# Kernel optimization log

Measured on AMD Instinct MI355X. Metric: run time of the kernel, lower is better.

Reference implementation:

```python
import jax, jax.numpy as jnp
import numpy as np

N = 8192
E = 524288
ALPHA = 0.4


def setup_inputs() -> dict:
    key = jax.random.key(0)
    k1, k2, k3, k4 = jax.random.split(key, 4)
    x = jax.random.normal(k1, (N, 64), dtype=jnp.float32)
    edge_attr = jax.random.uniform(k2, (E,), dtype=jnp.float32)
    row = jax.random.randint(k3, (E,), 0, N)
    col = jax.random.randint(k4, (E,), 0, N)
    edge_index = jnp.stack([row, col]).astype(jnp.int64)
    return {"x": x, "edge_attr": edge_attr, "edge_index": edge_index}


def reference(x, edge_attr, edge_index):
    # PPR diffusion: P = alpha*I + alpha*(1-alpha)*(A + A^2 + A^3)
    # (the theta *= (1-alpha) update in the torch loop is dead: spspmm reuses
    #  the already-scaled previous result, so all power terms share theta1)
    n = x.shape[0]
    row, col = edge_index[0], edge_index[1]
    # degree(col, N): unweighted in-degree count
    deg = jnp.zeros((n,), dtype=x.dtype).at[col].add(jnp.ones((), x.dtype))
    deg_inv_sqrt = deg ** -0.5  # inf at isolated nodes, matching torch pow(-0.5)
    vals = deg_inv_sqrt[row] * edge_attr * deg_inv_sqrt[col]
    # densify normalized adjacency (COO scatter-add == sparse coalesce semantics)
    A = jnp.zeros((n, n), dtype=x.dtype).at[row, col].add(vals)
    theta1 = ALPHA * (1.0 - ALPHA)
    A2 = A @ A      # [N,N]
    A3 = A @ A2     # [N,N]
    P = theta1 * (A + A2 + A3) + ALPHA * jnp.eye(n, dtype=x.dtype)
    return P
```

## Files before the change

### kernel.cpp

```cpp
#include <hip/hip_runtime.h>

#define NN 8192
#define ALPHA  0.4f
#define THETA1 0.24f
#define SLABW  128
#define NSLAB  (NN / SLABW)
#define SLABSZ ((size_t)NN * SLABW)

typedef float    f32x2 __attribute__((ext_vector_type(2)));
typedef float    f32x4 __attribute__((ext_vector_type(4)));
typedef unsigned u32x2 __attribute__((ext_vector_type(2)));

__device__ __forceinline__ unsigned short f2bf(float f) {
    unsigned u = __float_as_uint(f);
    u += 0x7fffu + ((u >> 16) & 1u);
    return (unsigned short)(u >> 16);
}

__global__ __launch_bounds__(256) void deg_count_kernel(const int* __restrict__ row,
                                                        const int* __restrict__ col,
                                                        float* __restrict__ deg,
                                                        int* __restrict__ cnt, int E) {
    int e = blockIdx.x * 256 + threadIdx.x;
    if (e >= E) return;
    unsigned r = (unsigned)row[e], c = (unsigned)col[e];
    if (r < NN && c < NN) {
        atomicAdd(&deg[c], 1.0f);
        atomicAdd(&cnt[r], 1);
    }
}

__global__ __launch_bounds__(256) void scan_kernel(const int* __restrict__ cnt,
                                                   int* __restrict__ rowptr,
                                                   int* __restrict__ cursor) {
    __shared__ int sums[257];
    int t = threadIdx.x;
    int base = t * 32;
    int s = 0;
    for (int j = 0; j < 32; ++j) s += cnt[base + j];
    sums[t] = s;
    __syncthreads();
    if (t == 0) {
        int run = 0;
        for (int i = 0; i < 256; ++i) { int x = sums[i]; sums[i] = run; run += x; }
        sums[256] = run;
    }
    __syncthreads();
    int run = sums[t];
    for (int j = 0; j < 32; ++j) {
        rowptr[base + j] = run;
        cursor[base + j] = run;
        run += cnt[base + j];
    }
    if (t == 255) rowptr[NN] = sums[256];
}

__global__ __launch_bounds__(256) void fill_kernel(const int* __restrict__ row,
                                                   const int* __restrict__ col,
                                                   const float* __restrict__ attr,
                                                   const float* __restrict__ deg,
                                                   int* __restrict__ cursor,
                                                   unsigned* __restrict__ epk,
                                                   float* __restrict__ Af, int E) {
    int e = blockIdx.x * 256 + threadIdx.x;
    if (e >= E) return;
    unsigned r = (unsigned)row[e], c = (unsigned)col[e];
    if (r < NN && c < NN) {
        float v = rsqrtf(deg[r]) * attr[e] * rsqrtf(deg[c]);
        atomicAdd(&Af[(size_t)r * NN + c], v);
        int pos = atomicAdd(&cursor[r], 1);
        epk[pos] = ((unsigned)f2bf(v) << 16) | c;
    }
}

__global__ __launch_bounds__(256) void convert_slab_kernel(const float* __restrict__ in,
                                                           unsigned short* __restrict__ out) {
    int r = blockIdx.x;
    int t = threadIdx.x;
    const float* rowp = in + (size_t)r * NN;
#pragma unroll
    for (int k = 0; k < 8; ++k) {
        int c = k * 1024 + t * 4;
        f32x4 v = __builtin_nontemporal_load((const f32x4*)&rowp[c]);
        unsigned lo = ((unsigned)f2bf(v.y) << 16) | (unsigned)f2bf(v.x);
        unsigned hi = ((unsigned)f2bf(v.w) << 16) | (unsigned)f2bf(v.z);
        u32x2 pk = {lo, hi};
        size_t o = (size_t)(c >> 7) * SLABSZ + (size_t)r * SLABW + (c & 127);
        __builtin_nontemporal_store(pk, (u32x2*)&out[o]);
    }
}

template <int FINAL>
__global__ __launch_bounds__(256) void spmm_kernel(const int* __restrict__ rowptr,
                                                   const unsigned* __restrict__ epk,
                                                   const unsigned short* __restrict__ S,
                                                   unsigned short* __restrict__ OutBf,
                                                   float* __restrict__ P,
                                                   const unsigned short* __restrict__ Abf,
                                                   const unsigned short* __restrict__ A2bf) {
    int lane = threadIdx.x & 63;
    int wave = threadIdx.x >> 6;
    unsigned bid   = blockIdx.x;
    unsigned xcd   = bid & 7u;
    unsigned local = bid >> 3;
    unsigned slab  = (xcd << 3) | (local >> 11);
    unsigned rg    = local & 2047u;
    int r  = (int)(rg * 4 + wave);
    int e0 = __builtin_amdgcn_readfirstlane(rowptr[r]);
    int e1 = __builtin_amdgcn_readfirstlane(rowptr[r + 1]);
    const char* Sc = (const char*)(S + (size_t)slab * SLABSZ) + (lane << 2);
    float a0 = 0.f, a1 = 0.f;

#define GATHER(u) (*(const unsigned*)(Sc + (((size_t)((u) & 0x1fffu)) << 8)))
#define ACCUM(g, u) { float vv = __uint_as_float((u) & 0xffff0000u);        \
                      a0 = fmaf(vv, __uint_as_float((g) << 16), a0);        \
                      a1 = fmaf(vv, __uint_as_float((g) & 0xffff0000u), a1); }
    int e = e0;
    for (; e + 8 <= e1; e += 8) {
        unsigned u0 = epk[e],     u1 = epk[e + 1];
        unsigned u2 = epk[e + 2], u3 = epk[e + 3];
        unsigned u4 = epk[e + 4], u5 = epk[e + 5];
        unsigned u6 = epk[e + 6], u7 = epk[e + 7];
        unsigned g0 = GATHER(u0), g1 = GATHER(u1), g2 = GATHER(u2), g3 = GATHER(u3);
        unsigned g4 = GATHER(u4), g5 = GATHER(u5), g6 = GATHER(u6), g7 = GATHER(u7);
        ACCUM(g0, u0); ACCUM(g1, u1); ACCUM(g2, u2); ACCUM(g3, u3);
        ACCUM(g4, u4); ACCUM(g5, u5); ACCUM(g6, u6); ACCUM(g7, u7);
    }
    for (; e < e1; ++e) {
        unsigned u = epk[e];
        unsigned g = GATHER(u);
        ACCUM(g, u);
    }
#undef GATHER
#undef ACCUM

    int cloc = lane << 1;
    size_t idx_sm = (size_t)slab * SLABSZ + (size_t)r * SLABW + cloc;
    if (FINAL) {
        unsigned ab = __builtin_nontemporal_load((const unsigned*)(Abf + idx_sm));
        unsigned bb = __builtin_nontemporal_load((const unsigned*)(A2bf + idx_sm));
        float o0 = THETA1 * (__uint_as_float(ab << 16) + __uint_as_float(bb << 16) + a0);
        float o1 = THETA1 * (__uint_as_float(ab & 0xffff0000u) + __uint_as_float(bb & 0xffff0000u) + a1);
        int gc = (int)(slab << 7) + cloc;
        int d = r - gc;
        if (d == 0) o0 += ALPHA;
        else if (d == 1) o1 += ALPHA;
        f32x2 o = {o0, o1};
        __builtin_nontemporal_store(o, (f32x2*)(P + (size_t)r * NN + gc));
    } else {
        unsigned pk = ((unsigned)f2bf(a1) << 16) | (unsigned)f2bf(a0);
        __builtin_nontemporal_store(pk, (unsigned*)(OutBf + idx_sm));
    }
}

extern "C" void kernel_launch(void* const* d_in, const int* in_sizes, int n_in,
                              void* d_out, int out_size, void* d_ws, size_t ws_size,
                              hipStream_t stream) {
    const float* attr = (const float*)d_in[1];
    const int*   eidx = (const int*)d_in[2];
    int E = in_sizes[1];
    const int* row = eidx;
    const int* col = eidx + E;

    const size_t MAT = (size_t)NN * NN;
    unsigned short* Abf  = (unsigned short*)d_ws;
    unsigned short* A2bf = Abf + MAT;
    float*    deg    = (float*)(A2bf + MAT);
    int*      cnt    = (int*)(deg + NN);
    int*      rowptr = cnt + NN;
    int*      cursor = rowptr + NN + 2;
    unsigned* epk    = (unsigned*)(cursor + NN);

    size_t need = MAT * 2 * sizeof(unsigned short)
                + (size_t)(NN * 4 + 2) * sizeof(int)
                + (size_t)E * sizeof(unsigned);
    if (ws_size < need) return;

    float* Af = (float*)d_out;
    float* P  = (float*)d_out;

    hipMemsetAsync(d_out, 0, MAT * sizeof(float), stream);
    hipMemsetAsync(deg, 0, NN * sizeof(float), stream);
    hipMemsetAsync(cnt, 0, NN * sizeof(int), stream);

    int eb = (E + 255) / 256;
    deg_count_kernel<<<eb, 256, 0, stream>>>(row, col, deg, cnt, E);
    scan_kernel<<<1, 256, 0, stream>>>(cnt, rowptr, cursor);
    fill_kernel<<<eb, 256, 0, stream>>>(row, col, attr, deg, cursor, epk, Af, E);
    convert_slab_kernel<<<NN, 256, 0, stream>>>(Af, Abf);

    const int SPMM_BLOCKS = 2048 * 64;
    spmm_kernel<0><<<SPMM_BLOCKS, 256, 0, stream>>>(rowptr, epk, Abf, A2bf, nullptr, nullptr, nullptr);
    spmm_kernel<1><<<SPMM_BLOCKS, 256, 0, stream>>>(rowptr, epk, A2bf, nullptr, P, Abf, A2bf);
}
```

Measured before the change: 1.279 ms.

## Factor PPR as A(I+A+A²) via Horner, split edges across half-waves

The first SpMM now writes S2 = I + A + A·A in bf16, and the final pass computes P = theta1·A·S2 + alpha·I. This removes the extra Abf and A2bf reads from the final kernel. Each wave is split into two 32-lane halves that take alternate edges and gather 8-byte chunks, and the halves are combined with a cross-half shuffle. The cost is an extra bf16 rounding of A+A² before the last product, and the upper half-wave is idle during the epilogue.

```diff
diff --git a/kernel.cpp b/kernel.cpp
--- a/kernel.cpp
+++ b/kernel.cpp
@@ -96,8 +96,7 @@
                                                    const unsigned short* __restrict__ S,
                                                    unsigned short* __restrict__ OutBf,
                                                    float* __restrict__ P,
-                                                   const unsigned short* __restrict__ Abf,
-                                                   const unsigned short* __restrict__ A2bf) {
+                                                   const unsigned short* __restrict__ Abf) {
     int lane = threadIdx.x & 63;
     int wave = threadIdx.x >> 6;
     unsigned bid   = blockIdx.x;
@@ -108,48 +107,81 @@
     int r  = (int)(rg * 4 + wave);
     int e0 = __builtin_amdgcn_readfirstlane(rowptr[r]);
     int e1 = __builtin_amdgcn_readfirstlane(rowptr[r + 1]);
-    const char* Sc = (const char*)(S + (size_t)slab * SLABSZ) + (lane << 2);
-    float a0 = 0.f, a1 = 0.f;
-
-#define GATHER(u) (*(const unsigned*)(Sc + (((size_t)((u) & 0x1fffu)) << 8)))
-#define ACCUM(g, u) { float vv = __uint_as_float((u) & 0xffff0000u);        \
-                      a0 = fmaf(vv, __uint_as_float((g) << 16), a0);        \
-                      a1 = fmaf(vv, __uint_as_float((g) & 0xffff0000u), a1); }
-    int e = e0;
-    for (; e + 8 <= e1; e += 8) {
-        unsigned u0 = epk[e],     u1 = epk[e + 1];
-        unsigned u2 = epk[e + 2], u3 = epk[e + 3];
-        unsigned u4 = epk[e + 4], u5 = epk[e + 5];
-        unsigned u6 = epk[e + 6], u7 = epk[e + 7];
-        unsigned g0 = GATHER(u0), g1 = GATHER(u1), g2 = GATHER(u2), g3 = GATHER(u3);
-        unsigned g4 = GATHER(u4), g5 = GATHER(u5), g6 = GATHER(u6), g7 = GATHER(u7);
-        ACCUM(g0, u0); ACCUM(g1, u1); ACCUM(g2, u2); ACCUM(g3, u3);
-        ACCUM(g4, u4); ACCUM(g5, u5); ACCUM(g6, u6); ACCUM(g7, u7);
-    }
-    for (; e < e1; ++e) {
-        unsigned u = epk[e];
-        unsigned g = GATHER(u);
-        ACCUM(g, u);
+    int hiHalf = lane >> 5;
+    int l32 = lane & 31;
+    const char* Sb = (const char*)(S + (size_t)slab * SLABSZ) + (l32 << 3);
+    float a0 = 0.f, a1 = 0.f, a2 = 0.f, a3 = 0.f;
+
+#define GATHER(u) (*(const u32x2*)(Sb + (((size_t)((u) & 0x1fffu)) << 8)))
+#define ACCUM4(g, u) { float vv = __uint_as_float((u) & 0xffff0000u);          \
+    a0 = fmaf(vv, __uint_as_float((g).x << 16), a0);                           \
+    a1 = fmaf(vv, __uint_as_float((g).x & 0xffff0000u), a1);                   \
+    a2 = fmaf(vv, __uint_as_float((g).y << 16), a2);                           \
+    a3 = fmaf(vv, __uint_as_float((g).y & 0xffff0000u), a3); }
+
+    const unsigned* ep = epk + e0;
+    int n = e1 - e0;
+    int npair = n >> 1;
+    int p = 0;
+    for (; p + 8 <= npair; p += 8) {
+        unsigned sel[8];
+#pragma unroll
+        for (int j = 0; j < 8; ++j) {
+            u32x2 q = *(const u32x2*)&ep[2 * (p + j)];
+            sel[j] = hiHalf ? q.y : q.x;
+        }
+        u32x2 g[8];
+#pragma unroll
+        for (int j = 0; j < 8; ++j) g[j] = GATHER(sel[j]);
+#pragma unroll
+        for (int j = 0; j < 8; ++j) ACCUM4(g[j], sel[j]);
+    }
+    for (; p < npair; ++p) {
+        u32x2 q = *(const u32x2*)&ep[2 * p];
+        unsigned s = hiHalf ? q.y : q.x;
+        u32x2 g = GATHER(s);
+        ACCUM4(g, s);
+    }
+    if (n & 1) {
+        unsigned u = ep[n - 1];
+        unsigned s = hiHalf ? 0u : u;
+        u32x2 g = GATHER(s);
+        ACCUM4(g, s);
     }
 #undef GATHER
-#undef ACCUM
-
-    int cloc = lane << 1;
+#undef ACCUM4
+
+    a0 += __shfl_xor(a0, 32);
+    a1 += __shfl_xor(a1, 32);
+    a2 += __shfl_xor(a2, 32);
+    a3 += __shfl_xor(a3, 32);
+    if (hiHalf) return;
+
+    int cloc = l32 << 2;
+    int gc   = (int)(slab << 7) + cloc;
+    int d    = r - gc;
     size_t idx_sm = (size_t)slab * SLABSZ + (size_t)r * SLABW + cloc;
     if (FINAL) {
-        unsigned ab = __builtin_nontemporal_load((const unsigned*)(Abf + idx_sm));
-        unsigned bb = __builtin_nontemporal_load((const unsigned*)(A2bf + idx_sm));
-        float o0 = THETA1 * (__uint_as_float(ab << 16) + __uint_as_float(bb << 16) + a0);
-        float o1 = THETA1 * (__uint_as_float(ab & 0xffff0000u) + __uint_as_float(bb & 0xffff0000u) + a1);
-        int gc = (int)(slab << 7) + cloc;
-        int d = r - gc;
+        float o0 = THETA1 * a0, o1 = THETA1 * a1, o2 = THETA1 * a2, o3 = THETA1 * a3;
         if (d == 0) o0 += ALPHA;
         else if (d == 1) o1 += ALPHA;
-        f32x2 o = {o0, o1};
-        __builtin_nontemporal_store(o, (f32x2*)(P + (size_t)r * NN + gc));
+        else if (d == 2) o2 += ALPHA;
+        else if (d == 3) o3 += ALPHA;
+        f32x4 o = {o0, o1, o2, o3};
+        __builtin_nontemporal_store(o, (f32x4*)(P + (size_t)r * NN + gc));
     } else {
-        unsigned pk = ((unsigned)f2bf(a1) << 16) | (unsigned)f2bf(a0);
-        __builtin_nontemporal_store(pk, (unsigned*)(OutBf + idx_sm));
+        u32x2 ab = __builtin_nontemporal_load((const u32x2*)(Abf + idx_sm));
+        float o0 = a0 + __uint_as_float(ab.x << 16);
+        float o1 = a1 + __uint_as_float(ab.x & 0xffff0000u);
+        float o2 = a2 + __uint_as_float(ab.y << 16);
+        float o3 = a3 + __uint_as_float(ab.y & 0xffff0000u);
+        if (d == 0) o0 += 1.0f;
+        else if (d == 1) o1 += 1.0f;
+        else if (d == 2) o2 += 1.0f;
+        else if (d == 3) o3 += 1.0f;
+        u32x2 pk = { (((unsigned)f2bf(o1)) << 16) | (unsigned)f2bf(o0),
+                     (((unsigned)f2bf(o3)) << 16) | (unsigned)f2bf(o2) };
+        __builtin_nontemporal_store(pk, (u32x2*)(OutBf + idx_sm));
     }
 }
 
@@ -164,8 +196,8 @@
 
     const size_t MAT = (size_t)NN * NN;
     unsigned short* Abf  = (unsigned short*)d_ws;
-    unsigned short* A2bf = Abf + MAT;
-    float*    deg    = (float*)(A2bf + MAT);
+    unsigned short* S2bf = Abf + MAT;
+    float*    deg    = (float*)(S2bf + MAT);
     int*      cnt    = (int*)(deg + NN);
     int*      rowptr = cnt + NN;
     int*      cursor = rowptr + NN + 2;
@@ -190,6 +222,6 @@
     convert_slab_kernel<<<NN, 256, 0, stream>>>(Af, Abf);
 
     const int SPMM_BLOCKS = 2048 * 64;
-    spmm_kernel<0><<<SPMM_BLOCKS, 256, 0, stream>>>(rowptr, epk, Abf, A2bf, nullptr, nullptr, nullptr);
-    spmm_kernel<1><<<SPMM_BLOCKS, 256, 0, stream>>>(rowptr, epk, A2bf, nullptr, P, Abf, A2bf);
-}
+    spmm_kernel<0><<<SPMM_BLOCKS, 256, 0, stream>>>(rowptr, epk, Abf, S2bf, nullptr, Abf);
+    spmm_kernel<1><<<SPMM_BLOCKS, 256, 0, stream>>>(rowptr, epk, S2bf, nullptr, P, nullptr);
+}
```

Result: slower. 1.467 ms (+14.8%).
